# Kernel optimization log

Measured on AMD Instinct MI355X. Metric: run time of the kernel, lower is better.

## Reference

```python
import jax, jax.numpy as jnp
import numpy as np

N, E = 50000, 800000
IN_CH, INTER, H1, H2 = 256, 32, 8, 8
C2 = IN_CH // H2  # 32
NEG_SLOPE = 0.2


def setup_inputs() -> dict:
    key = jax.random.key(0)
    ks = jax.random.split(key, 10)
    x = jax.random.normal(ks[0], (N, IN_CH), dtype=jnp.float32)
    edge_index = jax.random.randint(ks[1], (2, E), 0, N, dtype=jnp.int32)
    s = 0.05
    W1 = jax.random.normal(ks[2], (H1 * INTER, IN_CH), dtype=jnp.float32) * s
    att_src1 = jax.random.normal(ks[3], (1, H1, INTER), dtype=jnp.float32) * s
    att_dst1 = jax.random.normal(ks[4], (1, H1, INTER), dtype=jnp.float32) * s
    b1 = jnp.zeros((H1 * INTER,), dtype=jnp.float32)
    W2 = jax.random.normal(ks[5], (H2 * C2, H1 * INTER), dtype=jnp.float32) * s
    att_src2 = jax.random.normal(ks[6], (1, H2, C2), dtype=jnp.float32) * s
    att_dst2 = jax.random.normal(ks[7], (1, H2, C2), dtype=jnp.float32) * s
    b2 = jnp.zeros((H2 * C2,), dtype=jnp.float32)
    return {"x": x, "edge_index": edge_index,
            "W1": W1, "att_src1": att_src1, "att_dst1": att_dst1, "b1": b1,
            "W2": W2, "att_src2": att_src2, "att_dst2": att_dst2, "b2": b2}


def gat_conv(x, edge_index, W, att_src, att_dst, bias, H, C):
    # PyG GATConv (shared lin for src/dst, add_self_loops=False, concat=True)
    n = x.shape[0]
    src, dst = edge_index[0], edge_index[1]
    xw = (x @ W.T).reshape(n, H, C)                     # [N,H,C]
    a_src = jnp.sum(xw * att_src, axis=-1)              # [N,H]
    a_dst = jnp.sum(xw * att_dst, axis=-1)              # [N,H]
    e = a_src[src] + a_dst[dst]                         # [E,H]
    e = jnp.where(e >= 0, e, NEG_SLOPE * e)             # LeakyReLU(0.2)
    # segment softmax over edges grouped by destination node
    m = jax.ops.segment_max(e, dst, num_segments=n)     # [N,H]
    ex = jnp.exp(e - m[dst])
    denom = jax.ops.segment_sum(ex, dst, num_segments=n)
    alpha = ex / (denom[dst] + 1e-16)                   # [E,H]
    # weighted scatter-aggregate of source messages
    msg = xw[src] * alpha[:, :, None]                   # [E,H,C]
    out = jax.ops.segment_sum(msg, dst, num_segments=n) # [N,H,C]
    return out.reshape(n, H * C) + bias


def reference(x, edge_index, W1, att_src1, att_dst1, b1, W2, att_src2, att_dst2, b2):
    h = gat_conv(x, edge_index, W1, att_src1, att_dst1, b1, H1, INTER)
    h = jax.nn.gelu(h, approximate=False)  # F.gelu default is exact
    h = gat_conv(h, edge_index, W2, att_src2, att_dst2, b2, H2, C2)
    return h[-1]  # eval-path super node
```

## Files before the change

### kernel.cpp

```cpp
#include <hip/hip_runtime.h>
#include <math.h>

#define N_NODES 50000
#define N_EDGES 800000
#define TGT     (N_NODES - 1)
#define C2MAX   256
#define KCAP    258
#define ELMAX   256
#define ROWS    (ELMAX + 1)
#define PBLK    16
#define SCANBLK 1024

struct WS {
  int* cnt;
  int* cnt2;
  int* e2src;
  int* g_uniq;
  int* g_slot;
  int* g_misc;
  int* l1src;
  float* W1T;
  float* W2T;
  float* g_xw2;
  float* g_as2;
  float* g_ad2;
  float* g_as1;
  float* g_ad1;
  float* g_xw1;
};
__host__ __device__ inline WS carve(char* ws) {
  WS w; int* p = (int*)ws;
  w.cnt = p;    p += 16;
  w.cnt2 = p;   p += 272;
  w.e2src = p;  p += C2MAX;
  w.g_uniq = p; p += 272;
  w.g_slot = p; p += C2MAX;
  w.g_misc = p; p += 16;
  w.l1src = p;  p += KCAP * ELMAX;
  float* f = (float*)p;
  w.W1T = f;    f += 65536;
  w.W2T = f;    f += 65536;
  w.g_xw2 = f;  f += KCAP * 256;
  w.g_as2 = f;  f += KCAP * 8;
  w.g_ad2 = f;  f += KCAP * 8;
  w.g_as1 = f;  f += KCAP * ROWS * 8;
  w.g_ad1 = f;  f += KCAP * ROWS * 8;
  w.g_xw1 = f;
  return w;
}

__device__ void dedup_block(const int* e2src, int c2, int* s_e, int* s_scan,
                            int* s_uniq, int* s_slot, int* s_kv) {
  int t = threadIdx.x;
  if (t < c2) s_e[t] = e2src[t];
  __syncthreads();
  int s = 0, firstIdx = t;
  if (t < c2) {
    s = s_e[t];
    for (int q = 0; q < t; ++q) if (s_e[q] == s) { firstIdx = q; break; }
  }
  s_scan[t] = (t < c2 && firstIdx == t) ? 1 : 0;
  __syncthreads();
  for (int off = 1; off < 256; off <<= 1) {
    int add = (t >= off) ? s_scan[t - off] : 0;
    __syncthreads();
    s_scan[t] += add;
    __syncthreads();
  }
  if (t < c2 && firstIdx == t) s_uniq[s_scan[t] - 1] = s;
  __syncthreads();
  if (t < c2) s_slot[t] = s_scan[firstIdx] - 1;
  if (t == 0) {
    int K1 = (c2 > 0) ? s_scan[255] : 0;
    int kd = -1;
    for (int i = 0; i < K1; ++i) if (s_uniq[i] == TGT) { kd = i; break; }
    if (kd < 0) { s_uniq[K1] = TGT; kd = K1; K1++; }
    s_kv[0] = K1; s_kv[1] = kd;
  }
  __syncthreads();
}

__global__ __launch_bounds__(256) void k_scan2(const int* __restrict__ eidx,
    const float* __restrict__ W1, const float* __restrict__ W2, char* ws) {
  WS w = carve(ws);
  int tid = blockIdx.x * 256 + threadIdx.x;
  int nthreads = gridDim.x * 256;
  for (int i = tid; i < 65536; i += nthreads) {
    int o = i >> 8, c = i & 255;
    w.W1T[c * 256 + o] = W1[i];
    w.W2T[c * 256 + o] = W2[i];
  }
  const int* esrc = eidx;
  const int4* edst4 = (const int4*)(eidx + N_EDGES);
  for (int i = tid; i < N_EDGES / 4; i += nthreads) {
    int4 d = edst4[i];
    int dv[4] = {d.x, d.y, d.z, d.w};
#pragma unroll
    for (int j = 0; j < 4; ++j)
      if (dv[j] == TGT) {
        int p = atomicAdd(&w.cnt[0], 1);
        if (p < C2MAX) w.e2src[p] = esrc[4 * i + j];
      }
  }
}

__global__ __launch_bounds__(256) void k_scan1(const int* __restrict__ eidx, char* ws) {
  WS w = carve(ws);
  __shared__ int s_e[C2MAX], s_scan[256], s_uniq[KCAP], s_slot[C2MAX], s_kv[2];
  int c2 = min(w.cnt[0], C2MAX);
  dedup_block(w.e2src, c2, s_e, s_scan, s_uniq, s_slot, s_kv);
  int K1 = s_kv[0];
  if (blockIdx.x == 0) {
    int t = threadIdx.x;
    if (t < K1) w.g_uniq[t] = s_uniq[t];
    if (t < c2) w.g_slot[t] = s_slot[t];
    if (t == 0) { w.g_misc[0] = K1; w.g_misc[1] = s_kv[1]; }
  }
  int tid = blockIdx.x * 256 + threadIdx.x;
  int nthreads = gridDim.x * 256;
  const int* esrc = eidx;
  const int4* edst4 = (const int4*)(eidx + N_EDGES);
  for (int i = tid; i < N_EDGES / 4; i += nthreads) {
    int4 d = edst4[i];
    int dv[4] = {d.x, d.y, d.z, d.w};
#pragma unroll
    for (int j = 0; j < 4; ++j) {
      int k = -1;
      for (int q = 0; q < K1; ++q) if (s_uniq[q] == dv[j]) { k = q; break; }
      if (k >= 0) {
        int p = atomicAdd(&w.cnt2[k], 1);
        if (p < ELMAX) w.l1src[k * ELMAX + p] = esrc[4 * i + j];
      }
    }
  }
}

__global__ __launch_bounds__(256) void k_xw1(const float* __restrict__ x,
    const float* __restrict__ aS1, const float* __restrict__ aD1, char* ws) {
  WS w = carve(ws);
  int k = blockIdx.x;
  if (k >= w.g_misc[0]) return;
  int t = threadIdx.x;
  int ne = min(w.cnt2[k], ELMAX);
  int items = ne + 1;
  __shared__ __align__(16) float s_xsT[4 * 256];
  __shared__ float s_redS[4 * 256], s_redD[4 * 256];
  int myNode = w.g_uniq[k];

  for (int b = blockIdx.y; b * 4 < items; b += PBLK) {
    int base = b * 4;
    int na = min(4, items - base);
    for (int i = 0; i < na; ++i) {
      int it = base + i;
      int node = (it < ne) ? w.l1src[k * ELMAX + it] : myNode;
      s_xsT[t * 4 + i] = x[(size_t)node * 256 + t];
    }
    __syncthreads();
    float a0 = 0.f, a1 = 0.f, a2 = 0.f, a3 = 0.f;
#pragma unroll 16
    for (int c = 0; c < 256; ++c) {
      float wv = w.W1T[c * 256 + t];
      float4 xv = *(const float4*)&s_xsT[c * 4];
      a0 = fmaf(xv.x, wv, a0); a1 = fmaf(xv.y, wv, a1);
      a2 = fmaf(xv.z, wv, a2); a3 = fmaf(xv.w, wv, a3);
    }
    float accs[4] = {a0, a1, a2, a3};
    for (int i = 0; i < na; ++i) {
      int row = k * ROWS + base + i;
      w.g_xw1[(size_t)row * 256 + t] = accs[i];
      s_redS[i * 256 + t] = accs[i] * aS1[t];
      s_redD[i * 256 + t] = accs[i] * aD1[t];
    }
    __syncthreads();
    if (t < 32) {
      int i = t >> 3, h = t & 7;
      if (i < na) {
        float s = 0.f, dd = 0.f;
        for (int q = 0; q < 32; ++q) {
          s  += s_redS[i * 256 + h * 32 + q];
          dd += s_redD[i * 256 + h * 32 + q];
        }
        int row = k * ROWS + base + i;
        w.g_as1[row * 8 + h] = s;
        w.g_ad1[row * 8 + h] = dd;
      }
    }
    __syncthreads();
  }
}

__global__ __launch_bounds__(256) void k_attn(const float* __restrict__ b1,
    const float* __restrict__ aS2, const float* __restrict__ aD2, char* ws) {
  WS w = carve(ws);
  int k = blockIdx.x;
  if (k >= w.g_misc[0]) return;
  int t = threadIdx.x;
  int ne = min(w.cnt2[k], ELMAX);
  __shared__ float s_as[ROWS * 8];
  __shared__ float s_p[ELMAX * 8];
  __shared__ float s_den[8];
  __shared__ float s_h1[256];
  __shared__ float s_redS[256], s_redD[256];
  for (int i = t; i < (ne + 1) * 8; i += 256) s_as[i] = w.g_as1[(k * ROWS) * 8 + i];
  __syncthreads();
  if (t < 8) {
    int h = t;
    float adst = w.g_ad1[(k * ROWS + ne) * 8 + h];
    float m = -INFINITY;
    for (int j = 0; j < ne; ++j) {
      float e = s_as[j * 8 + h] + adst;
      e = (e >= 0.f) ? e : 0.2f * e;
      m = fmaxf(m, e);
    }
    float den = 0.f;
    for (int j = 0; j < ne; ++j) {
      float e = s_as[j * 8 + h] + adst;
      e = (e >= 0.f) ? e : 0.2f * e;
      float p = expf(e - m);
      s_p[j * 8 + h] = p;
      den += p;
    }
    s_den[h] = den + 1e-16f;
  }
  __syncthreads();
  int h = t >> 5;
  float acc = 0.f;
  const float* xwb = w.g_xw1 + (size_t)(k * ROWS) * 256 + t;
#pragma unroll 4
  for (int j = 0; j < ne; ++j)
    acc = fmaf(s_p[j * 8 + h], xwb[(size_t)j * 256], acc);
  float o = (ne > 0) ? acc / s_den[h] : 0.f;
  o += b1[t];
  s_h1[t] = 0.5f * o * (1.f + erff(o * 0.70710678118654752440f));
  __syncthreads();
  float a2s = 0.f;
#pragma unroll 16
  for (int c = 0; c < 256; ++c)
    a2s = fmaf(s_h1[c], w.W2T[c * 256 + t], a2s);
  w.g_xw2[k * 256 + t] = a2s;
  s_redS[t] = a2s * aS2[t];
  s_redD[t] = a2s * aD2[t];
  __syncthreads();
  if (t < 8) {
    float s = 0.f, dd = 0.f;
    for (int q = 0; q < 32; ++q) { s += s_redS[t * 32 + q]; dd += s_redD[t * 32 + q]; }
    w.g_as2[k * 8 + t] = s;
    w.g_ad2[k * 8 + t] = dd;
  }
}

__global__ __launch_bounds__(256) void k_final(const float* __restrict__ b2,
                                               float* __restrict__ out, char* ws) {
  WS w = carve(ws);
  int t = threadIdx.x;
  int c2 = min(w.cnt[0], C2MAX);
  int kd = w.g_misc[1];
  __shared__ int s_slot[C2MAX];
  __shared__ float s_p[C2MAX];
  __shared__ float s_den[8];
  if (t < c2) s_slot[t] = w.g_slot[t];
  __syncthreads();
  int h = t >> 5;
  if (t < 8) {
    float adst = w.g_ad2[kd * 8 + t];
    float m = -INFINITY;
    for (int j = 0; j < c2; ++j) {
      float e = w.g_as2[s_slot[j] * 8 + t] + adst;
      e = (e >= 0.f) ? e : 0.2f * e;
      m = fmaxf(m, e);
    }
    float den = 0.f;
    for (int j = 0; j < c2; ++j) {
      float e = w.g_as2[s_slot[j] * 8 + t] + adst;
      e = (e >= 0.f) ? e : 0.2f * e;
      den += expf(e - m);
    }
    s_den[t] = den + 1e-16f;
  }
  __syncthreads();
  if (t < 8) {
    float adst = w.g_ad2[kd * 8 + t];
    float m = -INFINITY;
    for (int j = 0; j < c2; ++j) {
      float e = w.g_as2[s_slot[j] * 8 + t] + adst;
      e = (e >= 0.f) ? e : 0.2f * e;
      m = fmaxf(m, e);
    }
    for (int j = 0; j < c2; ++j) {
      float e = w.g_as2[s_slot[j] * 8 + t] + adst;
      e = (e >= 0.f) ? e : 0.2f * e;
    }
  }
  __syncthreads();
  float adst = w.g_ad2[kd * 8 + h];
  float m = -INFINITY;
  for (int j = 0; j < c2; ++j) {
    float e = w.g_as2[s_slot[j] * 8 + h] + adst;
    e = (e >= 0.f) ? e : 0.2f * e;
    m = fmaxf(m, e);
  }
  float acc = 0.f;
  for (int j = 0; j < c2; ++j) {
    int kk = s_slot[j];
    float e = w.g_as2[kk * 8 + h] + adst;
    e = (e >= 0.f) ? e : 0.2f * e;
    float p = expf(e - m);
    acc = fmaf(p, w.g_xw2[kk * 256 + t], acc);
  }
  float o = (c2 > 0) ? acc / s_den[h] : 0.f;
  out[t] = o + b2[t];
}

extern "C" void kernel_launch(void* const* d_in, const int* in_sizes, int n_in,
                              void* d_out, int out_size, void* d_ws, size_t ws_size,
                              hipStream_t stream) {
  const float* x    = (const float*)d_in[0];
  const int*   eidx = (const int*)d_in[1];
  const float* W1   = (const float*)d_in[2];
  const float* aS1  = (const float*)d_in[3];
  const float* aD1  = (const float*)d_in[4];
  const float* b1   = (const float*)d_in[5];
  const float* W2   = (const float*)d_in[6];
  const float* aS2  = (const float*)d_in[7];
  const float* aD2  = (const float*)d_in[8];
  const float* b2   = (const float*)d_in[9];
  float* out = (float*)d_out;
  char*  ws  = (char*)d_ws;

  hipMemsetAsync(ws, 0, (16 + 272) * sizeof(int), stream);

  k_scan2<<<SCANBLK, 256, 0, stream>>>(eidx, W1, W2, ws);
  k_scan1<<<SCANBLK, 256, 0, stream>>>(eidx, ws);
  k_xw1  <<<dim3(KCAP, PBLK), 256, 0, stream>>>(x, aS1, aD1, ws);
  k_attn <<<KCAP, 256, 0, stream>>>(b1, aS2, aD2, ws);
  k_final<<<1, 256, 0, stream>>>(b2, out, ws);
}
```

Measured before the change: 142.9 us.

## Fuse xw1, attention and final stages with last-block-done atomics; add bitmap lookup

Merges the three per-node kernels into one launch. Per-node finalisation and the final output are handed to the last-arriving block, detected through agent-scope atomic counters. The destination-membership test in scan1 now uses a shared-memory bitmap before the linear search, which avoids a K1-long loop for most edges. W1/W2 are transposed through LDS tiles into a float4-interleaved layout so the GEMV loops can use vector loads. PBLK is halved, and the final softmax stores p once instead of recomputing the max and exp per thread. These changes save launch overhead and redundant work, but they rely on correct fences and add a serial tail at the end of the fused kernel.

Result: no change. 145.0 us (+1.5%).

```diff
diff --git a/kernel.cpp b/kernel.cpp
--- a/kernel.cpp
+++ b/kernel.cpp
@@ -8,19 +8,21 @@
 #define KCAP    258
 #define ELMAX   256
 #define ROWS    (ELMAX + 1)
-#define PBLK    16
+#define PBLK    8
 #define SCANBLK 1024
+#define BMWORDS 1568
 
 struct WS {
   int* cnt;
   int* cnt2;
+  int* fin_k;
   int* e2src;
   int* g_uniq;
   int* g_slot;
   int* g_misc;
   int* l1src;
-  float* W1T;
-  float* W2T;
+  float* W1T4;
+  float* W2T4;
   float* g_xw2;
   float* g_as2;
   float* g_ad2;
@@ -32,14 +34,15 @@
   WS w; int* p = (int*)ws;
   w.cnt = p;    p += 16;
   w.cnt2 = p;   p += 272;
+  w.fin_k = p;  p += 272;
   w.e2src = p;  p += C2MAX;
   w.g_uniq = p; p += 272;
   w.g_slot = p; p += C2MAX;
   w.g_misc = p; p += 16;
   w.l1src = p;  p += KCAP * ELMAX;
   float* f = (float*)p;
-  w.W1T = f;    f += 65536;
-  w.W2T = f;    f += 65536;
+  w.W1T4 = f;   f += 65536;
+  w.W2T4 = f;   f += 65536;
   w.g_xw2 = f;  f += KCAP * 256;
   w.g_as2 = f;  f += KCAP * 8;
   w.g_ad2 = f;  f += KCAP * 8;
@@ -49,47 +52,32 @@
   return w;
 }
 
-__device__ void dedup_block(const int* e2src, int c2, int* s_e, int* s_scan,
-                            int* s_uniq, int* s_slot, int* s_kv) {
-  int t = threadIdx.x;
-  if (t < c2) s_e[t] = e2src[t];
-  __syncthreads();
-  int s = 0, firstIdx = t;
-  if (t < c2) {
-    s = s_e[t];
-    for (int q = 0; q < t; ++q) if (s_e[q] == s) { firstIdx = q; break; }
-  }
-  s_scan[t] = (t < c2 && firstIdx == t) ? 1 : 0;
-  __syncthreads();
-  for (int off = 1; off < 256; off <<= 1) {
-    int add = (t >= off) ? s_scan[t - off] : 0;
-    __syncthreads();
-    s_scan[t] += add;
-    __syncthreads();
-  }
-  if (t < c2 && firstIdx == t) s_uniq[s_scan[t] - 1] = s;
-  __syncthreads();
-  if (t < c2) s_slot[t] = s_scan[firstIdx] - 1;
-  if (t == 0) {
-    int K1 = (c2 > 0) ? s_scan[255] : 0;
-    int kd = -1;
-    for (int i = 0; i < K1; ++i) if (s_uniq[i] == TGT) { kd = i; break; }
-    if (kd < 0) { s_uniq[K1] = TGT; kd = K1; K1++; }
-    s_kv[0] = K1; s_kv[1] = kd;
-  }
-  __syncthreads();
-}
-
 __global__ __launch_bounds__(256) void k_scan2(const int* __restrict__ eidx,
     const float* __restrict__ W1, const float* __restrict__ W2, char* ws) {
   WS w = carve(ws);
-  int tid = blockIdx.x * 256 + threadIdx.x;
+  int t = threadIdx.x;
+  __shared__ float lds[64][65];
+  if (blockIdx.x < 32) {
+    int m  = blockIdx.x >> 4;
+    int ti = (blockIdx.x >> 2) & 3, tj = blockIdx.x & 3;
+    const float* src = m ? W2 : W1;
+    float*       dst = m ? w.W2T4 : w.W1T4;
+    int r0 = t >> 6, cc = t & 63;
+    for (int p = 0; p < 16; ++p) {
+      int r = p * 4 + r0;
+      lds[r][cc] = src[(ti * 64 + r) * 256 + tj * 64 + cc];
+    }
+    __syncthreads();
+    int c40 = t >> 6, o = t & 63;
+    for (int p2 = 0; p2 < 4; ++p2) {
+      int c4l = p2 * 4 + c40;
+      float4 v = make_float4(lds[o][4 * c4l + 0], lds[o][4 * c4l + 1],
+                             lds[o][4 * c4l + 2], lds[o][4 * c4l + 3]);
+      ((float4*)dst)[(tj * 16 + c4l) * 256 + ti * 64 + o] = v;
+    }
+  }
+  int tid = blockIdx.x * 256 + t;
   int nthreads = gridDim.x * 256;
-  for (int i = tid; i < 65536; i += nthreads) {
-    int o = i >> 8, c = i & 255;
-    w.W1T[c * 256 + o] = W1[i];
-    w.W2T[c * 256 + o] = W2[i];
-  }
   const int* esrc = eidx;
   const int4* edst4 = (const int4*)(eidx + N_EDGES);
   for (int i = tid; i < N_EDGES / 4; i += nthreads) {
@@ -106,17 +94,49 @@
 
 __global__ __launch_bounds__(256) void k_scan1(const int* __restrict__ eidx, char* ws) {
   WS w = carve(ws);
+  int t = threadIdx.x;
   __shared__ int s_e[C2MAX], s_scan[256], s_uniq[KCAP], s_slot[C2MAX], s_kv[2];
+  __shared__ unsigned s_bm[BMWORDS];
   int c2 = min(w.cnt[0], C2MAX);
-  dedup_block(w.e2src, c2, s_e, s_scan, s_uniq, s_slot, s_kv);
+  if (t < c2) s_e[t] = w.e2src[t];
+  __syncthreads();
+  int firstIdx = t;
+  if (t < c2) {
+    int s = s_e[t];
+    for (int q = 0; q < t; ++q) if (s_e[q] == s) { firstIdx = q; break; }
+  }
+  s_scan[t] = (t < c2 && firstIdx == t) ? 1 : 0;
+  __syncthreads();
+  for (int off = 1; off < 256; off <<= 1) {
+    int add = (t >= off) ? s_scan[t - off] : 0;
+    __syncthreads();
+    s_scan[t] += add;
+    __syncthreads();
+  }
+  if (t < c2 && firstIdx == t) s_uniq[s_scan[t] - 1] = s_e[t];
+  __syncthreads();
+  if (t < c2) s_slot[t] = s_scan[firstIdx] - 1;
+  if (t == 0) {
+    int K1 = (c2 > 0) ? s_scan[255] : 0;
+    int kd = -1;
+    for (int i = 0; i < K1; ++i) if (s_uniq[i] == TGT) { kd = i; break; }
+    if (kd < 0) { s_uniq[K1] = TGT; kd = K1; K1++; }
+    s_kv[0] = K1; s_kv[1] = kd;
+  }
+  for (int i = t; i < BMWORDS; i += 256) s_bm[i] = 0u;
+  __syncthreads();
   int K1 = s_kv[0];
+  for (int i = t; i < K1; i += 256) {
+    int u = s_uniq[i];
+    atomicOr(&s_bm[u >> 5], 1u << (u & 31));
+  }
   if (blockIdx.x == 0) {
-    int t = threadIdx.x;
-    if (t < K1) w.g_uniq[t] = s_uniq[t];
+    for (int i = t; i < K1; i += 256) w.g_uniq[i] = s_uniq[i];
     if (t < c2) w.g_slot[t] = s_slot[t];
     if (t == 0) { w.g_misc[0] = K1; w.g_misc[1] = s_kv[1]; }
   }
-  int tid = blockIdx.x * 256 + threadIdx.x;
+  __syncthreads();
+  int tid = blockIdx.x * 256 + t;
   int nthreads = gridDim.x * 256;
   const int* esrc = eidx;
   const int4* edst4 = (const int4*)(eidx + N_EDGES);
@@ -125,9 +145,10 @@
     int dv[4] = {d.x, d.y, d.z, d.w};
 #pragma unroll
     for (int j = 0; j < 4; ++j) {
-      int k = -1;
-      for (int q = 0; q < K1; ++q) if (s_uniq[q] == dv[j]) { k = q; break; }
-      if (k >= 0) {
+      int u = dv[j];
+      if ((s_bm[u >> 5] >> (u & 31)) & 1u) {
+        int k = 0;
+        for (int q = 0; q < K1; ++q) if (s_uniq[q] == u) { k = q; break; }
         int p = atomicAdd(&w.cnt2[k], 1);
         if (p < ELMAX) w.l1src[k * ELMAX + p] = esrc[4 * i + j];
       }
@@ -135,17 +156,30 @@
   }
 }
 
-__global__ __launch_bounds__(256) void k_xw1(const float* __restrict__ x,
-    const float* __restrict__ aS1, const float* __restrict__ aD1, char* ws) {
+__global__ __launch_bounds__(256) void k_fused(const float* __restrict__ x,
+    const float* __restrict__ aS1, const float* __restrict__ aD1,
+    const float* __restrict__ b1, const float* __restrict__ aS2,
+    const float* __restrict__ aD2, const float* __restrict__ b2,
+    float* __restrict__ out, char* ws) {
   WS w = carve(ws);
+  int K1 = w.g_misc[0];
   int k = blockIdx.x;
-  if (k >= w.g_misc[0]) return;
+  if (k >= K1) return;
   int t = threadIdx.x;
   int ne = min(w.cnt2[k], ELMAX);
   int items = ne + 1;
+  int myNode = w.g_uniq[k];
   __shared__ __align__(16) float s_xsT[4 * 256];
   __shared__ float s_redS[4 * 256], s_redD[4 * 256];
-  int myNode = w.g_uniq[k];
+  __shared__ float s_as[ROWS * 8];
+  __shared__ float s_p[ELMAX * 8];
+  __shared__ float s_den[8];
+  __shared__ __align__(16) float s_h1[256];
+  __shared__ int   s_sl[C2MAX];
+  __shared__ int   s_win;
+  const float4* W1v = (const float4*)w.W1T4;
+  const float4* W2v = (const float4*)w.W2T4;
+  const float4* xsT4 = (const float4*)s_xsT;
 
   for (int b = blockIdx.y; b * 4 < items; b += PBLK) {
     int base = b * 4;
@@ -157,12 +191,17 @@
     }
     __syncthreads();
     float a0 = 0.f, a1 = 0.f, a2 = 0.f, a3 = 0.f;
-#pragma unroll 16
-    for (int c = 0; c < 256; ++c) {
-      float wv = w.W1T[c * 256 + t];
-      float4 xv = *(const float4*)&s_xsT[c * 4];
-      a0 = fmaf(xv.x, wv, a0); a1 = fmaf(xv.y, wv, a1);
-      a2 = fmaf(xv.z, wv, a2); a3 = fmaf(xv.w, wv, a3);
+#pragma unroll 8
+    for (int c4 = 0; c4 < 64; ++c4) {
+      float4 wv = W1v[c4 * 256 + t];
+      float4 x0 = xsT4[4 * c4 + 0];
+      float4 x1 = xsT4[4 * c4 + 1];
+      float4 x2 = xsT4[4 * c4 + 2];
+      float4 x3 = xsT4[4 * c4 + 3];
+      a0 = fmaf(wv.x, x0.x, a0); a0 = fmaf(wv.y, x1.x, a0); a0 = fmaf(wv.z, x2.x, a0); a0 = fmaf(wv.w, x3.x, a0);
+      a1 = fmaf(wv.x, x0.y, a1); a1 = fmaf(wv.y, x1.y, a1); a1 = fmaf(wv.z, x2.y, a1); a1 = fmaf(wv.w, x3.y, a1);
+      a2 = fmaf(wv.x, x0.z, a2); a2 = fmaf(wv.y, x1.z, a2); a2 = fmaf(wv.z, x2.z, a2); a2 = fmaf(wv.w, x3.z, a2);
+      a3 = fmaf(wv.x, x0.w, a3); a3 = fmaf(wv.y, x1.w, a3); a3 = fmaf(wv.z, x2.w, a3); a3 = fmaf(wv.w, x3.w, a3);
     }
     float accs[4] = {a0, a1, a2, a3};
     for (int i = 0; i < na; ++i) {
@@ -187,25 +226,23 @@
     }
     __syncthreads();
   }
-}
-
-__global__ __launch_bounds__(256) void k_attn(const float* __restrict__ b1,
-    const float* __restrict__ aS2, const float* __restrict__ aD2, char* ws) {
-  WS w = carve(ws);
-  int k = blockIdx.x;
-  if (k >= w.g_misc[0]) return;
-  int t = threadIdx.x;
-  int ne = min(w.cnt2[k], ELMAX);
-  __shared__ float s_as[ROWS * 8];
-  __shared__ float s_p[ELMAX * 8];
-  __shared__ float s_den[8];
-  __shared__ float s_h1[256];
-  __shared__ float s_redS[256], s_redD[256];
-  for (int i = t; i < (ne + 1) * 8; i += 256) s_as[i] = w.g_as1[(k * ROWS) * 8 + i];
+
+  __syncthreads();
+  if (t == 0) {
+    __threadfence();
+    int old = __hip_atomic_fetch_add(&w.fin_k[k], 1, __ATOMIC_ACQ_REL, __HIP_MEMORY_SCOPE_AGENT);
+    s_win = (old == PBLK - 1);
+  }
+  __syncthreads();
+  if (!s_win) return;
+  __threadfence();
+
+  for (int i = t; i < items * 8; i += 256) s_as[i] = w.g_as1[(size_t)(k * ROWS) * 8 + i];
   __syncthreads();
   if (t < 8) {
     int h = t;
-    float adst = w.g_ad1[(k * ROWS + ne) * 8 + h];
+    float adst = s_as[ne * 8 + h];
+    adst = w.g_ad1[(size_t)(k * ROWS + ne) * 8 + h];
     float m = -INFINITY;
     for (int j = 0; j < ne; ++j) {
       float e = s_as[j * 8 + h] + adst;
@@ -234,9 +271,14 @@
   s_h1[t] = 0.5f * o * (1.f + erff(o * 0.70710678118654752440f));
   __syncthreads();
   float a2s = 0.f;
-#pragma unroll 16
-  for (int c = 0; c < 256; ++c)
-    a2s = fmaf(s_h1[c], w.W2T[c * 256 + t], a2s);
+  const float4* h1v = (const float4*)s_h1;
+#pragma unroll 8
+  for (int c4 = 0; c4 < 64; ++c4) {
+    float4 wv = W2v[c4 * 256 + t];
+    float4 hv = h1v[c4];
+    a2s = fmaf(wv.x, hv.x, a2s); a2s = fmaf(wv.y, hv.y, a2s);
+    a2s = fmaf(wv.z, hv.z, a2s); a2s = fmaf(wv.w, hv.w, a2s);
+  }
   w.g_xw2[k * 256 + t] = a2s;
   s_redS[t] = a2s * aS2[t];
   s_redD[t] = a2s * aD2[t];
@@ -247,68 +289,45 @@
     w.g_as2[k * 8 + t] = s;
     w.g_ad2[k * 8 + t] = dd;
   }
-}
-
-__global__ __launch_bounds__(256) void k_final(const float* __restrict__ b2,
-                                               float* __restrict__ out, char* ws) {
-  WS w = carve(ws);
-  int t = threadIdx.x;
+
+  __syncthreads();
+  if (t == 0) {
+    __threadfence();
+    int old = __hip_atomic_fetch_add(&w.cnt[1], 1, __ATOMIC_ACQ_REL, __HIP_MEMORY_SCOPE_AGENT);
+    s_win = (old == K1 - 1);
+  }
+  __syncthreads();
+  if (!s_win) return;
+  __threadfence();
+
   int c2 = min(w.cnt[0], C2MAX);
   int kd = w.g_misc[1];
-  __shared__ int s_slot[C2MAX];
-  __shared__ float s_p[C2MAX];
-  __shared__ float s_den[8];
-  if (t < c2) s_slot[t] = w.g_slot[t];
-  __syncthreads();
-  int h = t >> 5;
+  for (int j = t; j < c2; j += 256) s_sl[j] = w.g_slot[j];
+  __syncthreads();
   if (t < 8) {
     float adst = w.g_ad2[kd * 8 + t];
     float m = -INFINITY;
     for (int j = 0; j < c2; ++j) {
-      float e = w.g_as2[s_slot[j] * 8 + t] + adst;
+      float e = w.g_as2[s_sl[j] * 8 + t] + adst;
       e = (e >= 0.f) ? e : 0.2f * e;
       m = fmaxf(m, e);
     }
     float den = 0.f;
     for (int j = 0; j < c2; ++j) {
-      float e = w.g_as2[s_slot[j] * 8 + t] + adst;
+      float e = w.g_as2[s_sl[j] * 8 + t] + adst;
       e = (e >= 0.f) ? e : 0.2f * e;
-      den += expf(e - m);
+      float p = expf(e - m);
+      s_p[j * 8 + t] = p;
+      den += p;
     }
     s_den[t] = den + 1e-16f;
   }
   __syncthreads();
-  if (t < 8) {
-    float adst = w.g_ad2[kd * 8 + t];
-    float m = -INFINITY;
-    for (int j = 0; j < c2; ++j) {
-      float e = w.g_as2[s_slot[j] * 8 + t] + adst;
-      e = (e >= 0.f) ? e : 0.2f * e;
-      m = fmaxf(m, e);
-    }
-    for (int j = 0; j < c2; ++j) {
-      float e = w.g_as2[s_slot[j] * 8 + t] + adst;
-      e = (e >= 0.f) ? e : 0.2f * e;
-    }
-  }
-  __syncthreads();
-  float adst = w.g_ad2[kd * 8 + h];
-  float m = -INFINITY;
-  for (int j = 0; j < c2; ++j) {
-    float e = w.g_as2[s_slot[j] * 8 + h] + adst;
-    e = (e >= 0.f) ? e : 0.2f * e;
-    m = fmaxf(m, e);
-  }
-  float acc = 0.f;
-  for (int j = 0; j < c2; ++j) {
-    int kk = s_slot[j];
-    float e = w.g_as2[kk * 8 + h] + adst;
-    e = (e >= 0.f) ? e : 0.2f * e;
-    float p = expf(e - m);
-    acc = fmaf(p, w.g_xw2[kk * 256 + t], acc);
-  }
-  float o = (c2 > 0) ? acc / s_den[h] : 0.f;
-  out[t] = o + b2[t];
+  float acc2 = 0.f;
+  for (int j = 0; j < c2; ++j)
+    acc2 = fmaf(s_p[j * 8 + h], w.g_xw2[s_sl[j] * 256 + t], acc2);
+  float o2 = (c2 > 0) ? acc2 / s_den[h] : 0.f;
+  out[t] = o2 + b2[t];
 }
 
 extern "C" void kernel_launch(void* const* d_in, const int* in_sizes, int n_in,
@@ -327,11 +346,9 @@
   float* out = (float*)d_out;
   char*  ws  = (char*)d_ws;
 
-  hipMemsetAsync(ws, 0, (16 + 272) * sizeof(int), stream);
+  hipMemsetAsync(ws, 0, (16 + 272 + 272) * sizeof(int), stream);
 
   k_scan2<<<SCANBLK, 256, 0, stream>>>(eidx, W1, W2, ws);
   k_scan1<<<SCANBLK, 256, 0, stream>>>(eidx, ws);
-  k_xw1  <<<dim3(KCAP, PBLK), 256, 0, stream>>>(x, aS1, aD1, ws);
-  k_attn <<<KCAP, 256, 0, stream>>>(b1, aS2, aD2, ws);
-  k_final<<<1, 256, 0, stream>>>(b2, out, ws);
-}
+  k_fused<<<dim3(KCAP, PBLK), 256, 0, stream>>>(x, aS1, aD1, b1, aS2, aD2, b2, out, ws);
+}
```
